# Performance work log

Measured on AMD Instinct MI355X. Metric: run time of the kernel, lower is better.

The kernel has to match this reference:

```python
import jax, jax.numpy as jnp
import numpy as np

B, S, H, P = 64, 2048, 1024, 8
MIN_BITS, MAX_BITS = 2.0, 8.0


def setup_inputs() -> dict:
    key = jax.random.key(0)
    k1, k2, k3 = jax.random.split(key, 3)
    return {
        "hidden_states": jax.random.normal(k1, (B, S, H), dtype=jnp.float32),
        "W1": 0.02 * jax.random.normal(k2, (H, H), dtype=jnp.float32),  # torch Linear: (out,in)
        "b1": jnp.zeros((H,), dtype=jnp.float32),
        "W2": 0.02 * jax.random.normal(k3, (P, H), dtype=jnp.float32),
        "b2": jnp.zeros((P,), dtype=jnp.float32),
        "temperature": jnp.ones((1,), dtype=jnp.float32),
        "total_budget": 32,
    }


def reference(hidden_states, W1, b1, W2, b2, temperature, total_budget):
    budget = jnp.float32(total_budget)
    # mean-pool over sequence: (B,S,H) -> (B,H); this dominates memory traffic
    pooled = hidden_states.mean(axis=1)
    h = jax.nn.silu(pooled @ W1.T + b1)          # (B,H)
    logits = h @ W2.T + b2                        # (B,P)
    temp = jnp.clip(temperature, 0.1, 5.0)
    attn_probs = jax.nn.softmax(logits / temp, axis=-1)
    # continuous bit allocation
    x = jnp.clip(attn_probs * budget, MIN_BITS, MAX_BITS)
    x = x * (budget / (x.sum(axis=-1, keepdims=True) + 1e-8))
    # straight-through round
    bits = jnp.round(x) - jax.lax.stop_gradient(x) + x  # numerically round(x)
    # vectorized exact-budget correction (torch loops per-sample with .item() syncs)
    diff = jax.lax.stop_gradient(jnp.trunc(budget - bits.sum(axis=-1)))  # (B,) int-valued, int() truncation
    idx = jnp.where(diff > 0, jnp.argmax(bits, axis=-1), jnp.argmin(bits, axis=-1))
    rows = jnp.arange(bits.shape[0])
    cur = bits[rows, idx]
    new = jnp.clip(cur + diff, MIN_BITS, MAX_BITS)
    bits = bits.at[rows, idx].set(jnp.where(diff != 0, new, cur))
    return bits, attn_probs
```

## Files before the change

kernel.cpp:

```cpp
#include <hip/hip_runtime.h>
#include <math.h>

#define BB 64
#define SS 2048
#define HH 1024
#define PP 8
#define SPLIT 16
#define ROWS (SS / SPLIT)

typedef float vf4 __attribute__((ext_vector_type(4)));

__global__ __launch_bounds__(256) void pool_partial_k(const float* __restrict__ hs,
                                                      float* __restrict__ part) {
    int blk = blockIdx.x;
    int b  = blk / SPLIT;
    int sp = blk % SPLIT;
    int t  = threadIdx.x;
    const vf4* base = reinterpret_cast<const vf4*>(
        hs + (size_t)b * SS * HH + (size_t)sp * ROWS * HH) + t;
    vf4 acc0 = (vf4)0.f, acc1 = (vf4)0.f, acc2 = (vf4)0.f, acc3 = (vf4)0.f;
    #pragma unroll 2
    for (int s = 0; s < ROWS; s += 4) {
        vf4 v0 = __builtin_nontemporal_load(&base[(size_t)(s + 0) * (HH / 4)]);
        vf4 v1 = __builtin_nontemporal_load(&base[(size_t)(s + 1) * (HH / 4)]);
        vf4 v2 = __builtin_nontemporal_load(&base[(size_t)(s + 2) * (HH / 4)]);
        vf4 v3 = __builtin_nontemporal_load(&base[(size_t)(s + 3) * (HH / 4)]);
        acc0 += v0; acc1 += v1; acc2 += v2; acc3 += v3;
    }
    reinterpret_cast<vf4*>(part)[(size_t)blk * (HH / 4) + t] =
        (acc0 + acc1) + (acc2 + acc3);
}

__global__ __launch_bounds__(512) void gemm_fused_k(const float* __restrict__ part,
                                                    const float* __restrict__ W1,
                                                    const float* __restrict__ b1,
                                                    float* __restrict__ hbuf) {
    int bg = blockIdx.x >> 4;
    int oc = blockIdx.x & 15;
    int t  = threadIdx.x;
    int wave = t >> 6, lane = t & 63;
    __shared__ vf4 spool[4][HH / 4];

    {
        int c  = t & 255;
        int r0 = t >> 8;
        #pragma unroll
        for (int rr = 0; rr < 2; ++rr) {
            int r = r0 + 2 * rr;
            int b = bg * 4 + r;
            const vf4* pb = reinterpret_cast<const vf4*>(part) +
                            (size_t)b * SPLIT * (HH / 4) + c;
            vf4 s = (vf4)0.f;
            #pragma unroll
            for (int sp = 0; sp < SPLIT; ++sp)
                s += pb[(size_t)sp * (HH / 4)];
            spool[r][c] = s * (1.0f / (float)SS);
        }
    }
    __syncthreads();

    int g = lane >> 4;
    int q = lane & 15;
    int o0 = oc * 64 + wave * 8 + g;
    int o1 = o0 + 4;
    const vf4* w0 = reinterpret_cast<const vf4*>(W1 + (size_t)o0 * HH) + q;
    const vf4* w1 = reinterpret_cast<const vf4*>(W1 + (size_t)o1 * HH) + q;
    float a0 = 0.f, a1 = 0.f, a2 = 0.f, a3 = 0.f;
    float c0 = 0.f, c1 = 0.f, c2 = 0.f, c3 = 0.f;
    #pragma unroll
    for (int k = 0; k < 16; ++k) {
        vf4 p0 = spool[0][q + 16 * k];
        vf4 p1 = spool[1][q + 16 * k];
        vf4 p2 = spool[2][q + 16 * k];
        vf4 p3 = spool[3][q + 16 * k];
        vf4 wa = w0[16 * k];
        vf4 wb = w1[16 * k];
        a0 += wa.x * p0.x + wa.y * p0.y + wa.z * p0.z + wa.w * p0.w;
        a1 += wa.x * p1.x + wa.y * p1.y + wa.z * p1.z + wa.w * p1.w;
        a2 += wa.x * p2.x + wa.y * p2.y + wa.z * p2.z + wa.w * p2.w;
        a3 += wa.x * p3.x + wa.y * p3.y + wa.z * p3.z + wa.w * p3.w;
        c0 += wb.x * p0.x + wb.y * p0.y + wb.z * p0.z + wb.w * p0.w;
        c1 += wb.x * p1.x + wb.y * p1.y + wb.z * p1.z + wb.w * p1.w;
        c2 += wb.x * p2.x + wb.y * p2.y + wb.z * p2.z + wb.w * p2.w;
        c3 += wb.x * p3.x + wb.y * p3.y + wb.z * p3.z + wb.w * p3.w;
    }
    #pragma unroll
    for (int off = 1; off < 16; off <<= 1) {
        a0 += __shfl_xor(a0, off); a1 += __shfl_xor(a1, off);
        a2 += __shfl_xor(a2, off); a3 += __shfl_xor(a3, off);
        c0 += __shfl_xor(c0, off); c1 += __shfl_xor(c1, off);
        c2 += __shfl_xor(c2, off); c3 += __shfl_xor(c3, off);
    }
    if (q < 4) {
        float sa = (q == 0) ? a0 : ((q == 1) ? a1 : ((q == 2) ? a2 : a3));
        float sc = (q == 0) ? c0 : ((q == 1) ? c1 : ((q == 2) ? c2 : c3));
        int b = bg * 4 + q;
        float za = sa + b1[o0];
        float zc = sc + b1[o1];
        hbuf[(size_t)b * HH + o0] = za / (1.f + expf(-za));
        hbuf[(size_t)b * HH + o1] = zc / (1.f + expf(-zc));
    }
}

__global__ __launch_bounds__(256) void head_k(const float* __restrict__ hbuf,
                                              const float* __restrict__ W2,
                                              const float* __restrict__ b2,
                                              const float* __restrict__ temp_p,
                                              const int* __restrict__ budget_p,
                                              float* __restrict__ out) {
    int b = blockIdx.x;
    int t = threadIdx.x;
    int wave = t >> 6, lane = t & 63;
    __shared__ float slog[PP];

    {
        const vf4* hrow = reinterpret_cast<const vf4*>(hbuf + (size_t)b * HH);
        int p0 = wave * 2, p1 = wave * 2 + 1;
        const vf4* w0 = reinterpret_cast<const vf4*>(W2 + (size_t)p0 * HH);
        const vf4* w1 = reinterpret_cast<const vf4*>(W2 + (size_t)p1 * HH);
        float s0 = 0.f, s1 = 0.f;
        #pragma unroll
        for (int k = 0; k < 4; ++k) {
            vf4 hv = hrow[lane + 64 * k];
            vf4 a = w0[lane + 64 * k];
            vf4 c = w1[lane + 64 * k];
            s0 += a.x * hv.x + a.y * hv.y + a.z * hv.z + a.w * hv.w;
            s1 += c.x * hv.x + c.y * hv.y + c.z * hv.z + c.w * hv.w;
        }
        #pragma unroll
        for (int off = 32; off; off >>= 1) {
            s0 += __shfl_xor(s0, off);
            s1 += __shfl_xor(s1, off);
        }
        if (lane == 0) {
            slog[p0] = s0 + b2[p0];
            slog[p1] = s1 + b2[p1];
        }
    }
    __syncthreads();
    if (wave != 0) return;

    float logit[PP];
    #pragma unroll
    for (int p = 0; p < PP; ++p) logit[p] = slog[p];
    float temp = fminf(fmaxf(temp_p[0], 0.1f), 5.0f);
    float budget = (float)budget_p[0];
    float inv_t = 1.0f / temp;
    float m = -INFINITY;
    #pragma unroll
    for (int p = 0; p < PP; ++p) { logit[p] *= inv_t; m = fmaxf(m, logit[p]); }
    float e[PP], se = 0.f;
    #pragma unroll
    for (int p = 0; p < PP; ++p) { e[p] = expf(logit[p] - m); se += e[p]; }
    float probs[PP];
    float inv_se = 1.0f / se;
    #pragma unroll
    for (int p = 0; p < PP; ++p) probs[p] = e[p] * inv_se;

    float x[PP], sx = 0.f;
    #pragma unroll
    for (int p = 0; p < PP; ++p) {
        x[p] = fminf(fmaxf(probs[p] * budget, 2.0f), 8.0f);
        sx += x[p];
    }
    float r = budget / (sx + 1e-8f);
    float bits[PP], sb = 0.f;
    #pragma unroll
    for (int p = 0; p < PP; ++p) {
        x[p] *= r;
        bits[p] = rintf(x[p]);
        sb += bits[p];
    }
    float diff = truncf(budget - sb);
    if (diff != 0.f) {
        int idx = 0;
        if (diff > 0.f) {
            float best = bits[0];
            for (int p = 1; p < PP; ++p) if (bits[p] > best) { best = bits[p]; idx = p; }
        } else {
            float best = bits[0];
            for (int p = 1; p < PP; ++p) if (bits[p] < best) { best = bits[p]; idx = p; }
        }
        bits[idx] = fminf(fmaxf(bits[idx] + diff, 2.0f), 8.0f);
    }

    if (t < PP)            out[b * PP + t] = bits[t];
    else if (t < 2 * PP)   out[BB * PP + b * PP + (t - PP)] = probs[t - PP];
}

extern "C" void kernel_launch(void* const* d_in, const int* in_sizes, int n_in,
                              void* d_out, int out_size, void* d_ws, size_t ws_size,
                              hipStream_t stream) {
    const float* hs     = (const float*)d_in[0];
    const float* W1     = (const float*)d_in[1];
    const float* b1     = (const float*)d_in[2];
    const float* W2     = (const float*)d_in[3];
    const float* b2     = (const float*)d_in[4];
    const float* temp   = (const float*)d_in[5];
    const int*   budget = (const int*)d_in[6];
    float* out = (float*)d_out;

    float* ws   = (float*)d_ws;
    float* part = ws;
    float* hbuf = ws + (size_t)BB * SPLIT * HH;

    hipLaunchKernelGGL(pool_partial_k, dim3(BB * SPLIT), dim3(256), 0, stream, hs, part);
    hipLaunchKernelGGL(gemm_fused_k,   dim3(256), dim3(512), 0, stream, part, W1, b1, hbuf);
    hipLaunchKernelGGL(head_k,         dim3(BB), dim3(256), 0, stream, hbuf, W2, b2, temp, budget, out);
}
```

Baseline: 107.2 us.

## Fuse head kernel into GEMM via last-block atomic counter; reshape pool unroll

Removes the separate head kernel launch. The last GEMM block to finish, found through an atomic counter reset at the start of the pool kernel, computes the W2 projection, softmax and bit allocation for all 64 rows. The pooling loop also moves from four accumulators to two with a higher unroll. This saves a launch and its gap, but the head work now runs serially in a single block and adds threadfence and atomic overhead.

```diff
diff --git a/kernel.cpp b/kernel.cpp
--- a/kernel.cpp
+++ b/kernel.cpp
@@ -7,39 +7,49 @@
 #define PP 8
 #define SPLIT 16
 #define ROWS (SS / SPLIT)
+#define GEMM_BLOCKS 256
 
 typedef float vf4 __attribute__((ext_vector_type(4)));
 
 __global__ __launch_bounds__(256) void pool_partial_k(const float* __restrict__ hs,
-                                                      float* __restrict__ part) {
+                                                      float* __restrict__ part,
+                                                      unsigned int* __restrict__ done) {
+    if (blockIdx.x == 0 && threadIdx.x == 0) atomicExch(done, 0u);
     int blk = blockIdx.x;
     int b  = blk / SPLIT;
     int sp = blk % SPLIT;
     int t  = threadIdx.x;
     const vf4* base = reinterpret_cast<const vf4*>(
         hs + (size_t)b * SS * HH + (size_t)sp * ROWS * HH) + t;
-    vf4 acc0 = (vf4)0.f, acc1 = (vf4)0.f, acc2 = (vf4)0.f, acc3 = (vf4)0.f;
-    #pragma unroll 2
-    for (int s = 0; s < ROWS; s += 4) {
+    vf4 acc0 = (vf4)0.f;
+    vf4 acc1 = (vf4)0.f;
+    #pragma unroll 4
+    for (int s = 0; s < ROWS; s += 2) {
         vf4 v0 = __builtin_nontemporal_load(&base[(size_t)(s + 0) * (HH / 4)]);
         vf4 v1 = __builtin_nontemporal_load(&base[(size_t)(s + 1) * (HH / 4)]);
-        vf4 v2 = __builtin_nontemporal_load(&base[(size_t)(s + 2) * (HH / 4)]);
-        vf4 v3 = __builtin_nontemporal_load(&base[(size_t)(s + 3) * (HH / 4)]);
-        acc0 += v0; acc1 += v1; acc2 += v2; acc3 += v3;
-    }
-    reinterpret_cast<vf4*>(part)[(size_t)blk * (HH / 4) + t] =
-        (acc0 + acc1) + (acc2 + acc3);
+        acc0 += v0;
+        acc1 += v1;
+    }
+    reinterpret_cast<vf4*>(part)[(size_t)blk * (HH / 4) + t] = acc0 + acc1;
 }
 
 __global__ __launch_bounds__(512) void gemm_fused_k(const float* __restrict__ part,
                                                     const float* __restrict__ W1,
                                                     const float* __restrict__ b1,
-                                                    float* __restrict__ hbuf) {
+                                                    const float* __restrict__ W2,
+                                                    const float* __restrict__ b2,
+                                                    const float* __restrict__ temp_p,
+                                                    const int* __restrict__ budget_p,
+                                                    float* __restrict__ hbuf,
+                                                    float* __restrict__ out,
+                                                    unsigned int* __restrict__ done) {
     int bg = blockIdx.x >> 4;
     int oc = blockIdx.x & 15;
     int t  = threadIdx.x;
     int wave = t >> 6, lane = t & 63;
     __shared__ vf4 spool[4][HH / 4];
+    __shared__ float slog[BB][PP];
+    __shared__ unsigned int slast;
 
     {
         int c  = t & 255;
@@ -59,133 +69,134 @@
     }
     __syncthreads();
 
-    int g = lane >> 4;
-    int q = lane & 15;
-    int o0 = oc * 64 + wave * 8 + g;
-    int o1 = o0 + 4;
-    const vf4* w0 = reinterpret_cast<const vf4*>(W1 + (size_t)o0 * HH) + q;
-    const vf4* w1 = reinterpret_cast<const vf4*>(W1 + (size_t)o1 * HH) + q;
-    float a0 = 0.f, a1 = 0.f, a2 = 0.f, a3 = 0.f;
-    float c0 = 0.f, c1 = 0.f, c2 = 0.f, c3 = 0.f;
-    #pragma unroll
-    for (int k = 0; k < 16; ++k) {
-        vf4 p0 = spool[0][q + 16 * k];
-        vf4 p1 = spool[1][q + 16 * k];
-        vf4 p2 = spool[2][q + 16 * k];
-        vf4 p3 = spool[3][q + 16 * k];
-        vf4 wa = w0[16 * k];
-        vf4 wb = w1[16 * k];
-        a0 += wa.x * p0.x + wa.y * p0.y + wa.z * p0.z + wa.w * p0.w;
-        a1 += wa.x * p1.x + wa.y * p1.y + wa.z * p1.z + wa.w * p1.w;
-        a2 += wa.x * p2.x + wa.y * p2.y + wa.z * p2.z + wa.w * p2.w;
-        a3 += wa.x * p3.x + wa.y * p3.y + wa.z * p3.z + wa.w * p3.w;
-        c0 += wb.x * p0.x + wb.y * p0.y + wb.z * p0.z + wb.w * p0.w;
-        c1 += wb.x * p1.x + wb.y * p1.y + wb.z * p1.z + wb.w * p1.w;
-        c2 += wb.x * p2.x + wb.y * p2.y + wb.z * p2.z + wb.w * p2.w;
-        c3 += wb.x * p3.x + wb.y * p3.y + wb.z * p3.z + wb.w * p3.w;
-    }
-    #pragma unroll
-    for (int off = 1; off < 16; off <<= 1) {
-        a0 += __shfl_xor(a0, off); a1 += __shfl_xor(a1, off);
-        a2 += __shfl_xor(a2, off); a3 += __shfl_xor(a3, off);
-        c0 += __shfl_xor(c0, off); c1 += __shfl_xor(c1, off);
-        c2 += __shfl_xor(c2, off); c3 += __shfl_xor(c3, off);
-    }
-    if (q < 4) {
-        float sa = (q == 0) ? a0 : ((q == 1) ? a1 : ((q == 2) ? a2 : a3));
-        float sc = (q == 0) ? c0 : ((q == 1) ? c1 : ((q == 2) ? c2 : c3));
-        int b = bg * 4 + q;
-        float za = sa + b1[o0];
-        float zc = sc + b1[o1];
-        hbuf[(size_t)b * HH + o0] = za / (1.f + expf(-za));
-        hbuf[(size_t)b * HH + o1] = zc / (1.f + expf(-zc));
-    }
-}
-
-__global__ __launch_bounds__(256) void head_k(const float* __restrict__ hbuf,
-                                              const float* __restrict__ W2,
-                                              const float* __restrict__ b2,
-                                              const float* __restrict__ temp_p,
-                                              const int* __restrict__ budget_p,
-                                              float* __restrict__ out) {
-    int b = blockIdx.x;
-    int t = threadIdx.x;
-    int wave = t >> 6, lane = t & 63;
-    __shared__ float slog[PP];
-
-    {
-        const vf4* hrow = reinterpret_cast<const vf4*>(hbuf + (size_t)b * HH);
-        int p0 = wave * 2, p1 = wave * 2 + 1;
-        const vf4* w0 = reinterpret_cast<const vf4*>(W2 + (size_t)p0 * HH);
-        const vf4* w1 = reinterpret_cast<const vf4*>(W2 + (size_t)p1 * HH);
-        float s0 = 0.f, s1 = 0.f;
-        #pragma unroll
-        for (int k = 0; k < 4; ++k) {
-            vf4 hv = hrow[lane + 64 * k];
-            vf4 a = w0[lane + 64 * k];
-            vf4 c = w1[lane + 64 * k];
-            s0 += a.x * hv.x + a.y * hv.y + a.z * hv.z + a.w * hv.w;
-            s1 += c.x * hv.x + c.y * hv.y + c.z * hv.z + c.w * hv.w;
-        }
-        #pragma unroll
-        for (int off = 32; off; off >>= 1) {
-            s0 += __shfl_xor(s0, off);
-            s1 += __shfl_xor(s1, off);
-        }
-        if (lane == 0) {
-            slog[p0] = s0 + b2[p0];
-            slog[p1] = s1 + b2[p1];
-        }
-    }
-    __syncthreads();
+    {
+        int g = lane >> 4;
+        int q = lane & 15;
+        int o0 = oc * 64 + wave * 8 + g;
+        int o1 = o0 + 4;
+        const vf4* w0 = reinterpret_cast<const vf4*>(W1 + (size_t)o0 * HH) + q;
+        const vf4* w1 = reinterpret_cast<const vf4*>(W1 + (size_t)o1 * HH) + q;
+        float a0 = 0.f, a1 = 0.f, a2 = 0.f, a3 = 0.f;
+        float c0 = 0.f, c1 = 0.f, c2 = 0.f, c3 = 0.f;
+        #pragma unroll
+        for (int k = 0; k < 16; ++k) {
+            vf4 p0 = spool[0][q + 16 * k];
+            vf4 p1 = spool[1][q + 16 * k];
+            vf4 p2 = spool[2][q + 16 * k];
+            vf4 p3 = spool[3][q + 16 * k];
+            vf4 wa = w0[16 * k];
+            vf4 wb = w1[16 * k];
+            a0 += wa.x * p0.x + wa.y * p0.y + wa.z * p0.z + wa.w * p0.w;
+            a1 += wa.x * p1.x + wa.y * p1.y + wa.z * p1.z + wa.w * p1.w;
+            a2 += wa.x * p2.x + wa.y * p2.y + wa.z * p2.z + wa.w * p2.w;
+            a3 += wa.x * p3.x + wa.y * p3.y + wa.z * p3.z + wa.w * p3.w;
+            c0 += wb.x * p0.x + wb.y * p0.y + wb.z * p0.z + wb.w * p0.w;
+            c1 += wb.x * p1.x + wb.y * p1.y + wb.z * p1.z + wb.w * p1.w;
+            c2 += wb.x * p2.x + wb.y * p2.y + wb.z * p2.z + wb.w * p2.w;
+            c3 += wb.x * p3.x + wb.y * p3.y + wb.z * p3.z + wb.w * p3.w;
+        }
+        #pragma unroll
+        for (int off = 1; off < 16; off <<= 1) {
+            a0 += __shfl_xor(a0, off); a1 += __shfl_xor(a1, off);
+            a2 += __shfl_xor(a2, off); a3 += __shfl_xor(a3, off);
+            c0 += __shfl_xor(c0, off); c1 += __shfl_xor(c1, off);
+            c2 += __shfl_xor(c2, off); c3 += __shfl_xor(c3, off);
+        }
+        if (q < 4) {
+            float sa = (q == 0) ? a0 : ((q == 1) ? a1 : ((q == 2) ? a2 : a3));
+            float sc = (q == 0) ? c0 : ((q == 1) ? c1 : ((q == 2) ? c2 : c3));
+            int b = bg * 4 + q;
+            float za = sa + b1[o0];
+            float zc = sc + b1[o1];
+            hbuf[(size_t)b * HH + o0] = za / (1.f + expf(-za));
+            hbuf[(size_t)b * HH + o1] = zc / (1.f + expf(-zc));
+        }
+    }
+
+    __threadfence();
+    __syncthreads();
+    if (t == 0) {
+        unsigned int old = atomicAdd(done, 1u);
+        slast = (old == GEMM_BLOCKS - 1) ? 1u : 0u;
+        if (slast) atomicExch(done, 0u);
+    }
+    __syncthreads();
+    if (!slast) return;
+    __threadfence();
+
+    {
+        int p = lane >> 3, q = lane & 7;
+        const vf4* w2r = reinterpret_cast<const vf4*>(W2 + (size_t)p * HH) + q * 32;
+        for (int bb = 0; bb < 8; ++bb) {
+            int b = wave * 8 + bb;
+            const vf4* hr = reinterpret_cast<const vf4*>(hbuf + (size_t)b * HH) + q * 32;
+            float s = 0.f;
+            #pragma unroll
+            for (int j = 0; j < 32; ++j) {
+                vf4 hv = hr[j];
+                vf4 wv = w2r[j];
+                s += wv.x * hv.x + wv.y * hv.y + wv.z * hv.z + wv.w * hv.w;
+            }
+            s += __shfl_xor(s, 1);
+            s += __shfl_xor(s, 2);
+            s += __shfl_xor(s, 4);
+            if (q == 0) slog[b][p] = s + b2[p];
+        }
+    }
+    __syncthreads();
+
     if (wave != 0) return;
-
-    float logit[PP];
-    #pragma unroll
-    for (int p = 0; p < PP; ++p) logit[p] = slog[p];
-    float temp = fminf(fmaxf(temp_p[0], 0.1f), 5.0f);
-    float budget = (float)budget_p[0];
-    float inv_t = 1.0f / temp;
-    float m = -INFINITY;
-    #pragma unroll
-    for (int p = 0; p < PP; ++p) { logit[p] *= inv_t; m = fmaxf(m, logit[p]); }
-    float e[PP], se = 0.f;
-    #pragma unroll
-    for (int p = 0; p < PP; ++p) { e[p] = expf(logit[p] - m); se += e[p]; }
-    float probs[PP];
-    float inv_se = 1.0f / se;
-    #pragma unroll
-    for (int p = 0; p < PP; ++p) probs[p] = e[p] * inv_se;
-
-    float x[PP], sx = 0.f;
-    #pragma unroll
-    for (int p = 0; p < PP; ++p) {
-        x[p] = fminf(fmaxf(probs[p] * budget, 2.0f), 8.0f);
-        sx += x[p];
-    }
-    float r = budget / (sx + 1e-8f);
-    float bits[PP], sb = 0.f;
-    #pragma unroll
-    for (int p = 0; p < PP; ++p) {
-        x[p] *= r;
-        bits[p] = rintf(x[p]);
-        sb += bits[p];
-    }
-    float diff = truncf(budget - sb);
-    if (diff != 0.f) {
-        int idx = 0;
-        if (diff > 0.f) {
-            float best = bits[0];
-            for (int p = 1; p < PP; ++p) if (bits[p] > best) { best = bits[p]; idx = p; }
-        } else {
-            float best = bits[0];
-            for (int p = 1; p < PP; ++p) if (bits[p] < best) { best = bits[p]; idx = p; }
-        }
-        bits[idx] = fminf(fmaxf(bits[idx] + diff, 2.0f), 8.0f);
-    }
-
-    if (t < PP)            out[b * PP + t] = bits[t];
-    else if (t < 2 * PP)   out[BB * PP + b * PP + (t - PP)] = probs[t - PP];
+    {
+        int b = lane;
+        float logit[PP];
+        #pragma unroll
+        for (int p = 0; p < PP; ++p) logit[p] = slog[b][p];
+        float temp = fminf(fmaxf(temp_p[0], 0.1f), 5.0f);
+        float budget = (float)budget_p[0];
+        float inv_t = 1.0f / temp;
+        float m = -INFINITY;
+        #pragma unroll
+        for (int p = 0; p < PP; ++p) { logit[p] *= inv_t; m = fmaxf(m, logit[p]); }
+        float e[PP], se = 0.f;
+        #pragma unroll
+        for (int p = 0; p < PP; ++p) { e[p] = expf(logit[p] - m); se += e[p]; }
+        float probs[PP];
+        float inv_se = 1.0f / se;
+        #pragma unroll
+        for (int p = 0; p < PP; ++p) probs[p] = e[p] * inv_se;
+
+        float x[PP], sx = 0.f;
+        #pragma unroll
+        for (int p = 0; p < PP; ++p) {
+            x[p] = fminf(fmaxf(probs[p] * budget, 2.0f), 8.0f);
+            sx += x[p];
+        }
+        float r = budget / (sx + 1e-8f);
+        float bits[PP], sb = 0.f;
+        #pragma unroll
+        for (int p = 0; p < PP; ++p) {
+            x[p] *= r;
+            bits[p] = rintf(x[p]);
+            sb += bits[p];
+        }
+        float diff = truncf(budget - sb);
+        if (diff != 0.f) {
+            int idx = 0;
+            if (diff > 0.f) {
+                float best = bits[0];
+                for (int p = 1; p < PP; ++p) if (bits[p] > best) { best = bits[p]; idx = p; }
+            } else {
+                float best = bits[0];
+                for (int p = 1; p < PP; ++p) if (bits[p] < best) { best = bits[p]; idx = p; }
+            }
+            bits[idx] = fminf(fmaxf(bits[idx] + diff, 2.0f), 8.0f);
+        }
+        #pragma unroll
+        for (int p = 0; p < PP; ++p) {
+            out[b * PP + p] = bits[p];
+            out[BB * PP + b * PP + p] = probs[p];
+        }
+    }
 }
 
 extern "C" void kernel_launch(void* const* d_in, const int* in_sizes, int n_in,
@@ -203,8 +214,9 @@
     float* ws   = (float*)d_ws;
     float* part = ws;
     float* hbuf = ws + (size_t)BB * SPLIT * HH;
-
-    hipLaunchKernelGGL(pool_partial_k, dim3(BB * SPLIT), dim3(256), 0, stream, hs, part);
-    hipLaunchKernelGGL(gemm_fused_k,   dim3(256), dim3(512), 0, stream, part, W1, b1, hbuf);
-    hipLaunchKernelGGL(head_k,         dim3(BB), dim3(256), 0, stream, hbuf, W2, b2, temp, budget, out);
+    unsigned int* done = (unsigned int*)(ws + (size_t)BB * SPLIT * HH + (size_t)BB * HH + 64);
+
+    hipLaunchKernelGGL(pool_partial_k, dim3(BB * SPLIT), dim3(256), 0, stream, hs, part, done);
+    hipLaunchKernelGGL(gemm_fused_k,   dim3(GEMM_BLOCKS), dim3(512), 0, stream,
+                       part, W1, b1, W2, b2, temp, budget, hbuf, out, done);
 }
```

New measurement: 199.0 us. 1.86x slower.
